# Performance work log

Measured on AMD Instinct MI355X. Metric: run time of the kernel, lower is better.

## Reference

```python
import jax, jax.numpy as jnp
import numpy as np

B, S, D, E = 8, 4096, 2048, 8
CHUNK = 128
TAU = 0.7


def setup_inputs() -> dict:
    key = jax.random.key(0)
    k0, k1, k2 = jax.random.split(key, 3)
    H = D // 2
    x = jax.random.normal(k0, (B, S, D), dtype=jnp.float32)
    W1 = jax.random.normal(k1, (D, H), dtype=jnp.float32) * (1.0 / np.sqrt(D))
    b1 = jnp.zeros((H,), dtype=jnp.float32)
    W2 = jax.random.normal(k2, (H, E), dtype=jnp.float32) * (1.0 / np.sqrt(H))
    b2 = jnp.zeros((E,), dtype=jnp.float32)
    return {"x": x, "W1": W1, "b1": b1, "W2": W2, "b2": b2}


def reference(x, W1, b1, W2, b2):
    b, s, d = x.shape
    e = W2.shape[1]
    c = s // CHUNK  # num_chunks (seq_len divisible by chunk_size)
    # router MLP: Linear -> ReLU -> Linear
    logits = jnp.maximum(x @ W1 + b1, 0.0) @ W2 + b2  # [B,S,E]
    # per-chunk mean logits
    chunk_logits = logits.reshape(b, c, CHUNK, e).mean(axis=2)  # [B,C,E]
    bidx = jnp.arange(b)
    # chunk 0: plain argmax
    init = jnp.argmax(chunk_logits[:, 0], axis=-1)  # [B]
    # chunks 1..C-1: hysteresis recurrence via scan
    def step(prev, cl):  # cl: [B,E]
        ce = jnp.argmax(cl, axis=-1)
        diff = cl[bidx, ce] - cl[bidx, prev]
        new = jnp.where(diff > TAU, ce, prev)
        return new, new
    _, rest = jax.lax.scan(step, init, jnp.swapaxes(chunk_logits[:, 1:], 0, 1))
    expert_indices = jnp.concatenate([init[:, None], rest.T], axis=1)  # [B,C]
    oh = jax.nn.one_hot(expert_indices, e, dtype=logits.dtype)  # [B,C,E]
    routing_weights = jnp.broadcast_to(oh[:, :, None, :], (b, c, CHUNK, e)).reshape(b, s, e)
    return routing_weights, expert_indices
```

## Files before the change

### kernel.cpp

```cpp
#include <hip/hip_runtime.h>

typedef unsigned int uint;
typedef unsigned short ushort;

#define BB 8
#define SS 4096
#define DD 2048
#define HH 1024
#define EE 8
#define CHUNK 128
#define NCHUNK 32
#define TAU 0.7f

#define BM 128
#define BN 256
#define BK 32
#define KITERS (DD / BK)
#define NSLICE (HH / BN)

typedef short bf16x8 __attribute__((ext_vector_type(8)));
typedef float f32x16 __attribute__((ext_vector_type(16)));

__device__ inline uint pack_rn(float a, float b) {
    uint ua = __float_as_uint(a), ub = __float_as_uint(b);
    ua += 0x7FFFu + ((ua >> 16) & 1u);
    ub += 0x7FFFu + ((ub >> 16) & 1u);
    return (ua >> 16) | (ub & 0xFFFF0000u);
}

__global__ __launch_bounds__(256) void reorder_w1_kernel(
    const float* __restrict__ W1, ushort* __restrict__ w1b)
{
    const int kg = blockIdx.x >> 2;
    const int n  = ((blockIdx.x & 3) << 8) + threadIdx.x;
    float v[8];
#pragma unroll
    for (int j = 0; j < 8; ++j) v[j] = W1[(size_t)(kg * 8 + j) * HH + n];
    uint pk[4];
#pragma unroll
    for (int p = 0; p < 4; ++p) pk[p] = pack_rn(v[2 * p], v[2 * p + 1]);
    const size_t off = (size_t)kg * HH + n;
    ((uint4*)w1b)[off] = make_uint4(pk[0], pk[1], pk[2], pk[3]);
}

__global__ __launch_bounds__(256, 2) void router_gemm_kernel(
    const float* __restrict__ x,
    const ushort* __restrict__ w1b,
    const float* __restrict__ b1,
    const float* __restrict__ W2,
    float* __restrict__ chunk_logits)
{
    const int bid   = blockIdx.x;
    const int xcd   = bid & 7;
    const int loc   = bid >> 3;
    const int bc    = xcd * 32 + (loc >> 2);
    const int slice = loc & 3;
    const int n0    = slice * BN;

    const int tid  = threadIdx.x;
    const int wave = tid >> 6;
    const int lane = tid & 63;
    const int lm   = lane & 31;
    const int kq   = lane >> 5;
    const int wn   = wave * 64;

    __shared__ __align__(16) float  As_f[2][4][2][BM][4];
    __shared__ __align__(16) ushort Bs[2][4][BN][8];
    __shared__ float  W2s[BN][EE];
    __shared__ float  b1s[BN];
    __shared__ float  red[4][EE];

    const float* xrow = x + (size_t)bc * CHUNK * DD;

    ((float4*)&W2s[0][0])[tid]       = ((const float4*)(W2 + (size_t)n0 * EE))[tid];
    ((float4*)&W2s[0][0])[tid + 256] = ((const float4*)(W2 + (size_t)n0 * EE))[tid + 256];
    if (tid < BN / 4) ((float4*)b1s)[tid] = ((const float4*)(b1 + n0))[tid];

    f32x16 acc[4][2];
#pragma unroll
    for (int i = 0; i < 4; ++i)
#pragma unroll
        for (int j = 0; j < 2; ++j)
#pragma unroll
            for (int r = 0; r < 16; ++r) acc[i][j][r] = 0.0f;

#define STAGE(tp, buf) do {                                                          \
        _Pragma("unroll")                                                            \
        for (int i = 0; i < 4; ++i) {                                               \
            const int half_ = i >> 1;                                                \
            const int mrow_ = (i & 1) * 64 + lane;                                   \
            const float* gsrc_ = xrow + (size_t)mrow_ * DD                           \
                                 + ((tp) * BK + wave * 8 + half_ * 4);               \
            __builtin_amdgcn_global_load_lds(                                        \
                (const __attribute__((address_space(1))) uint*)gsrc_,                \
                (__attribute__((address_space(3))) uint*)&As_f[buf][wave][half_][mrow_][0], \
                16, 0, 0);                                                           \
        }                                                                            \
        {                                                                            \
            const int kgg_ = (tp) * 4 + wave;                                        \
            _Pragma("unroll")                                                        \
            for (int h = 0; h < 4; ++h) {                                            \
                const size_t goff_ = ((size_t)kgg_ * HH + n0 + h * 64 + lane) * 8;   \
                __builtin_amdgcn_global_load_lds(                                    \
                    (const __attribute__((address_space(1))) uint*)(w1b + goff_),    \
                    (__attribute__((address_space(3))) uint*)&Bs[buf][wave][h * 64 + lane][0], \
                    16, 0, 0);                                                       \
            }                                                                        \
        }                                                                            \
    } while (0)

#define MFMA_PHASE(buf) do {                                                         \
        _Pragma("unroll")                                                            \
        for (int s = 0; s < 2; ++s) {                                                \
            const int kg = 2 * s + kq;                                               \
            bf16x8 a[4], b[2];                                                       \
            _Pragma("unroll")                                                        \
            for (int i = 0; i < 4; ++i) {                                            \
                const float4 lo = *(const float4*)&As_f[buf][kg][0][i * 32 + lm][0]; \
                const float4 hi = *(const float4*)&As_f[buf][kg][1][i * 32 + lm][0]; \
                uint4 pk4 = make_uint4(pack_rn(lo.x, lo.y), pack_rn(lo.z, lo.w),     \
                                       pack_rn(hi.x, hi.y), pack_rn(hi.z, hi.w));    \
                a[i] = *(bf16x8*)&pk4;                                               \
            }                                                                        \
            _Pragma("unroll")                                                        \
            for (int j = 0; j < 2; ++j)                                              \
                b[j] = *(const bf16x8*)&Bs[buf][kg][wn + j * 32 + lm][0];            \
            __builtin_amdgcn_s_setprio(1);                                           \
            _Pragma("unroll")                                                        \
            for (int i = 0; i < 4; ++i)                                              \
                _Pragma("unroll")                                                    \
                for (int j = 0; j < 2; ++j)                                          \
                    acc[i][j] = __builtin_amdgcn_mfma_f32_32x32x16_bf16(             \
                        a[i], b[j], acc[i][j], 0, 0, 0);                             \
            __builtin_amdgcn_s_setprio(0);                                           \
        }                                                                            \
    } while (0)

    STAGE(0, 0);
    asm volatile("s_waitcnt vmcnt(0)" ::: "memory");
    __builtin_amdgcn_s_barrier();
    asm volatile("" ::: "memory");

    for (int t = 0; t < KITERS - 1; ++t) {
        const int cur = t & 1;
        STAGE(t + 1, cur ^ 1);
        asm volatile("s_waitcnt vmcnt(8)" ::: "memory");
        __builtin_amdgcn_s_barrier();
        asm volatile("" ::: "memory");
        MFMA_PHASE(cur);
        asm volatile("s_waitcnt lgkmcnt(0)" ::: "memory");
        __builtin_amdgcn_s_barrier();
        asm volatile("" ::: "memory");
    }
    asm volatile("s_waitcnt vmcnt(0)" ::: "memory");
    __builtin_amdgcn_s_barrier();
    asm volatile("" ::: "memory");
    MFMA_PHASE((KITERS - 1) & 1);

    float part[EE];
#pragma unroll
    for (int e = 0; e < EE; ++e) part[e] = 0.0f;

#pragma unroll
    for (int j = 0; j < 2; ++j) {
        const int hl = wn + j * 32 + lm;
        const float bias = b1s[hl];
        float w2r[EE];
#pragma unroll
        for (int e = 0; e < EE; ++e) w2r[e] = W2s[hl][e];
#pragma unroll
        for (int i = 0; i < 4; ++i)
#pragma unroll
            for (int r = 0; r < 16; ++r) {
                const float hv = fmaxf(acc[i][j][r] + bias, 0.0f);
#pragma unroll
                for (int e = 0; e < EE; ++e) part[e] = fmaf(hv, w2r[e], part[e]);
            }
    }

#pragma unroll
    for (int off = 32; off >= 1; off >>= 1)
#pragma unroll
        for (int e = 0; e < EE; ++e) part[e] += __shfl_down(part[e], off, 64);

    if (lane == 0)
#pragma unroll
        for (int e = 0; e < EE; ++e) red[wave][e] = part[e];
    __syncthreads();
    if (tid < EE) {
        const float s = red[0][tid] + red[1][tid] + red[2][tid] + red[3][tid];
        atomicAdd(&chunk_logits[(size_t)bc * EE + tid], s * (1.0f / CHUNK));
    }
}

__global__ __launch_bounds__(256) void finalize_kernel(
    const float* __restrict__ chunk_logits,
    const float* __restrict__ b2,
    float* __restrict__ out)
{
    __shared__ float cls[NCHUNK][EE];
    __shared__ int   idxs[NCHUNK];
    const int tid = threadIdx.x;
    const int b   = blockIdx.x >> 4;
    const int sg  = blockIdx.x & 15;

    {
        const int c = tid >> 3, e = tid & 7;
        cls[c][e] = chunk_logits[(size_t)(b * NCHUNK + c) * EE + e] + b2[e];
    }
    __syncthreads();

    if (tid == 0) {
        int prev = 0;
        for (int c = 0; c < NCHUNK; ++c) {
            float best = -3.4e38f;
            int ce = 0;
#pragma unroll
            for (int e = 0; e < EE; ++e) {
                const float lv = cls[c][e];
                if (lv > best) { best = lv; ce = e; }
            }
            if (c == 0) prev = ce;
            else if (best - cls[c][prev] > TAU) prev = ce;
            idxs[c] = prev;
        }
    }
    __syncthreads();

    const int tok = sg * 256 + tid;
    const int id  = idxs[tok >> 7];
    float v[EE];
#pragma unroll
    for (int e = 0; e < EE; ++e) v[e] = (e == id) ? 1.0f : 0.0f;
    float4* o = (float4*)(out + ((size_t)b * SS + tok) * EE);
    o[0] = make_float4(v[0], v[1], v[2], v[3]);
    o[1] = make_float4(v[4], v[5], v[6], v[7]);

    if (sg == 0 && tid < NCHUNK)
        out[(size_t)BB * SS * EE + b * NCHUNK + tid] = (float)idxs[tid];
}

extern "C" void kernel_launch(void* const* d_in, const int* in_sizes, int n_in,
                              void* d_out, int out_size, void* d_ws, size_t ws_size,
                              hipStream_t stream)
{
    const float* x  = (const float*)d_in[0];
    const float* W1 = (const float*)d_in[1];
    const float* b1 = (const float*)d_in[2];
    const float* W2 = (const float*)d_in[3];
    const float* b2 = (const float*)d_in[4];
    float* out = (float*)d_out;

    ushort* w1b          = (ushort*)d_ws;
    float*  chunk_logits = (float*)((char*)d_ws + (size_t)8 * 1024 * 1024);

    hipMemsetAsync(chunk_logits, 0, BB * NCHUNK * EE * sizeof(float), stream);

    reorder_w1_kernel<<<1024, 256, 0, stream>>>(W1, w1b);

    router_gemm_kernel<<<NSLICE * BB * NCHUNK, 256, 0, stream>>>(
        x, w1b, b1, W2, chunk_logits);

    finalize_kernel<<<BB * 16, 256, 0, stream>>>(chunk_logits, b2, out);
}
```

Measured before the change: 595.8 us.

## Convert x tiles to bf16 once in registers before writing to LDS

```diff
diff --git a/kernel.cpp b/kernel.cpp
--- a/kernel.cpp
+++ b/kernel.cpp
@@ -64,7 +64,7 @@
     const int kq   = lane >> 5;
     const int wn   = wave * 64;
 
-    __shared__ __align__(16) float  As_f[2][4][2][BM][4];
+    __shared__ __align__(16) ushort As[2][4][BM][8];
     __shared__ __align__(16) ushort Bs[2][4][BN][8];
     __shared__ float  W2s[BN][EE];
     __shared__ float  b1s[BN];
@@ -84,29 +84,31 @@
 #pragma unroll
             for (int r = 0; r < 16; ++r) acc[i][j][r] = 0.0f;
 
-#define STAGE(tp, buf) do {                                                          \
+    const int am = tid >> 1;
+    const int ah = tid & 1;
+    const float* asrc = xrow + (size_t)am * DD + ah * 16;
+
+#define STAGE_B(tp, buf) do {                                                        \
+        const int kgg_ = (tp) * 4 + wave;                                            \
         _Pragma("unroll")                                                            \
-        for (int i = 0; i < 4; ++i) {                                               \
-            const int half_ = i >> 1;                                                \
-            const int mrow_ = (i & 1) * 64 + lane;                                   \
-            const float* gsrc_ = xrow + (size_t)mrow_ * DD                           \
-                                 + ((tp) * BK + wave * 8 + half_ * 4);               \
+        for (int h = 0; h < 4; ++h) {                                                \
+            const size_t goff_ = ((size_t)kgg_ * HH + n0 + h * 64 + lane) * 8;       \
             __builtin_amdgcn_global_load_lds(                                        \
-                (const __attribute__((address_space(1))) uint*)gsrc_,                \
-                (__attribute__((address_space(3))) uint*)&As_f[buf][wave][half_][mrow_][0], \
+                (const __attribute__((address_space(1))) uint*)(w1b + goff_),        \
+                (__attribute__((address_space(3))) uint*)&Bs[buf][wave][h * 64 + lane][0], \
                 16, 0, 0);                                                           \
         }                                                                            \
-        {                                                                            \
-            const int kgg_ = (tp) * 4 + wave;                                        \
-            _Pragma("unroll")                                                        \
-            for (int h = 0; h < 4; ++h) {                                            \
-                const size_t goff_ = ((size_t)kgg_ * HH + n0 + h * 64 + lane) * 8;   \
-                __builtin_amdgcn_global_load_lds(                                    \
-                    (const __attribute__((address_space(1))) uint*)(w1b + goff_),    \
-                    (__attribute__((address_space(3))) uint*)&Bs[buf][wave][h * 64 + lane][0], \
-                    16, 0, 0);                                                       \
-            }                                                                        \
-        }                                                                            \
+    } while (0)
+
+#define WRITE_A(v0, v1, v2, v3, buf) do {                                            \
+        const float f_[16] = {v0.x, v0.y, v0.z, v0.w, v1.x, v1.y, v1.z, v1.w,        \
+                              v2.x, v2.y, v2.z, v2.w, v3.x, v3.y, v3.z, v3.w};       \
+        uint pk_[8];                                                                 \
+        _Pragma("unroll")                                                            \
+        for (int p = 0; p < 8; ++p) pk_[p] = pack_rn(f_[2 * p], f_[2 * p + 1]);      \
+        const int kg0_ = ah * 2;                                                     \
+        *(uint4*)&As[buf][kg0_][am][0]     = make_uint4(pk_[0], pk_[1], pk_[2], pk_[3]); \
+        *(uint4*)&As[buf][kg0_ + 1][am][0] = make_uint4(pk_[4], pk_[5], pk_[6], pk_[7]); \
     } while (0)
 
 #define MFMA_PHASE(buf) do {                                                         \
@@ -115,13 +117,8 @@
             const int kg = 2 * s + kq;                                               \
             bf16x8 a[4], b[2];                                                       \
             _Pragma("unroll")                                                        \
-            for (int i = 0; i < 4; ++i) {                                            \
-                const float4 lo = *(const float4*)&As_f[buf][kg][0][i * 32 + lm][0]; \
-                const float4 hi = *(const float4*)&As_f[buf][kg][1][i * 32 + lm][0]; \
-                uint4 pk4 = make_uint4(pack_rn(lo.x, lo.y), pack_rn(lo.z, lo.w),     \
-                                       pack_rn(hi.x, hi.y), pack_rn(hi.z, hi.w));    \
-                a[i] = *(bf16x8*)&pk4;                                               \
-            }                                                                        \
+            for (int i = 0; i < 4; ++i)                                              \
+                a[i] = *(const bf16x8*)&As[buf][kg][i * 32 + lm][0];                 \
             _Pragma("unroll")                                                        \
             for (int j = 0; j < 2; ++j)                                              \
                 b[j] = *(const bf16x8*)&Bs[buf][kg][wn + j * 32 + lm][0];            \
@@ -136,25 +133,28 @@
         }                                                                            \
     } while (0)
 
-    STAGE(0, 0);
-    asm volatile("s_waitcnt vmcnt(0)" ::: "memory");
-    __builtin_amdgcn_s_barrier();
-    asm volatile("" ::: "memory");
+    {
+        float4 v0 = ((const float4*)asrc)[0];
+        float4 v1 = ((const float4*)asrc)[1];
+        float4 v2 = ((const float4*)asrc)[2];
+        float4 v3 = ((const float4*)asrc)[3];
+        STAGE_B(0, 0);
+        WRITE_A(v0, v1, v2, v3, 0);
+    }
+    __syncthreads();
 
     for (int t = 0; t < KITERS - 1; ++t) {
         const int cur = t & 1;
-        STAGE(t + 1, cur ^ 1);
-        asm volatile("s_waitcnt vmcnt(8)" ::: "memory");
-        __builtin_amdgcn_s_barrier();
-        asm volatile("" ::: "memory");
+        STAGE_B(t + 1, cur ^ 1);
+        const float* s2 = asrc + (size_t)(t + 1) * BK;
+        float4 v0 = ((const float4*)s2)[0];
+        float4 v1 = ((const float4*)s2)[1];
+        float4 v2 = ((const float4*)s2)[2];
+        float4 v3 = ((const float4*)s2)[3];
         MFMA_PHASE(cur);
-        asm volatile("s_waitcnt lgkmcnt(0)" ::: "memory");
-        __builtin_amdgcn_s_barrier();
-        asm volatile("" ::: "memory");
-    }
-    asm volatile("s_waitcnt vmcnt(0)" ::: "memory");
-    __builtin_amdgcn_s_barrier();
-    asm volatile("" ::: "memory");
+        WRITE_A(v0, v1, v2, v3, cur ^ 1);
+        __syncthreads();
+    }
     MFMA_PHASE((KITERS - 1) & 1);
 
     float part[EE];
```

Measured after the change: 579.8 us. 1.03x faster.
